# Optimization experiments

Measured on AMD Instinct MI355X. Metric: run time of the kernel, lower is better.

Reference implementation:

```python
import jax, jax.numpy as jnp
import numpy as np

DIM_IN, DIM_OUT, DIM_CTX = 128, 256, 259
B, N, S_CTX = 32, 2048, 1
BN_EPS = 1e-5


def setup_inputs() -> dict:
    key = jax.random.key(0)
    ks = jax.random.split(key, 12)
    s = 0.02
    return {
        "ctx": jax.random.normal(ks[0], (B, S_CTX, DIM_CTX), jnp.float32),
        "x": jax.random.normal(ks[1], (B, N, DIM_IN), jnp.float32),
        "W_layer": jax.random.normal(ks[2], (DIM_OUT, DIM_IN), jnp.float32) * s,
        "b_layer": jax.random.normal(ks[3], (DIM_OUT,), jnp.float32) * s,
        "W_hbias": jax.random.normal(ks[4], (DIM_OUT, DIM_CTX), jnp.float32) * s,
        "W_gate": jax.random.normal(ks[5], (DIM_OUT, DIM_CTX), jnp.float32) * s,
        "b_gate": jax.random.normal(ks[6], (DIM_OUT,), jnp.float32) * s,
        "W_k": jax.random.normal(ks[7], (DIM_OUT, DIM_CTX - 3), jnp.float32) * s,
        "W_v": jax.random.normal(ks[8], (DIM_OUT, DIM_CTX - 3), jnp.float32) * s,
        "W_tc": jax.random.normal(ks[9], (DIM_OUT, DIM_OUT), jnp.float32) * s,
        "b_tc": jax.random.normal(ks[10], (DIM_OUT,), jnp.float32) * s,
        "bn_gamma": jnp.ones((N,), jnp.float32),
        "bn_beta": jnp.zeros((N,), jnp.float32),
    }


def reference(ctx, x, W_layer, b_layer, W_hbias, W_gate, b_gate, W_k, W_v, W_tc, b_tc, bn_gamma, bn_beta):
    # FiLM gate / bias from context: [B, 1, dim_out]
    gate = jax.nn.sigmoid(jnp.einsum('bsc,oc->bso', ctx, W_gate) + b_gate)
    bias = jnp.einsum('bsc,oc->bso', ctx, W_hbias)

    # main linear: [B, N, dim_out]
    x1 = jnp.einsum('bni,oi->bno', x, W_layer) + b_layer

    # channel attention from shape context (drop last 3 ctx dims)
    shape = ctx[:, :, : ctx.shape[2] - 3]                      # [B, S, C-3]
    shape_k = jnp.einsum('bsc,oc->bos', shape, W_k)            # [B, dim_out, S]
    shape_v = jnp.einsum('bsc,oc->bso', shape, W_v)            # [B, S, dim_out]
    energy = jnp.einsum('bos,bse->boe', shape_k, shape_v)      # [B, dim_out, dim_out]
    attention = jax.nn.softmax(energy, axis=-1)
    attention = attention / (1e-9 + attention.sum(axis=1, keepdims=True))

    # channel mixing: [B, N, dim_out]
    x_r = jnp.einsum('bno,boe->bne', x1, attention)

    # trans_conv + BatchNorm1d(N) (train-mode batch stats over dims (0, 2)) + ReLU
    t = jnp.einsum('bno,eo->bne', x1 - x_r, W_tc) + b_tc       # [B, N, dim_out]
    mean = t.mean(axis=(0, 2), keepdims=True)                  # per point-channel
    var = t.var(axis=(0, 2), keepdims=True)                    # biased variance
    t = (t - mean) * jax.lax.rsqrt(var + BN_EPS)
    t = t * bn_gamma[None, :, None] + bn_beta[None, :, None]
    x_r = jax.nn.relu(t)

    xo = x1 + x_r
    return xo * gate + bias
```

## Files before the change

kernel.cpp:

```cpp
#include <hip/hip_runtime.h>
#include <hip/hip_bf16.h>

#define BB   32
#define NN   2048
#define DIN  128
#define DOUT 256
#define DCTX 259

#define OFF_AB   0u
#define OFF_WMB  16777216u
#define OFF_WLB  17301504u
#define OFF_WLTB 17317888u
#define OFF_WTCB 17334272u
#define OFF_G    17367040u
#define OFF_HB   17375232u
#define OFF_TB   17383424u
#define OFF_WKT  17391616u
#define OFF_WVT  17457152u
#define OFF_WGT  17522688u
#define OFF_WHT  17588992u
#define OFF_P1   17655296u
#define OFF_P2   17720832u
#define OFF_SC   17786368u
#define OFF_SH   17788416u

typedef short bf16x8 __attribute__((ext_vector_type(8)));
typedef float f32x4  __attribute__((ext_vector_type(4)));

static __device__ inline unsigned short f2bf(float f) {
    __hip_bfloat16 h = __float2bfloat16(f);
    return *(unsigned short*)&h;
}
static __device__ inline float bf2f(unsigned short u) {
    unsigned v = ((unsigned)u) << 16;
    float f;
    __builtin_memcpy(&f, &v, 4);
    return f;
}

__global__ void kXW(const float* __restrict__ Wl, const float* __restrict__ Wtc,
                    const float* __restrict__ Wk, const float* __restrict__ Wv,
                    const float* __restrict__ Wg, const float* __restrict__ Whb,
                    float* __restrict__ ws) {
    unsigned bb = blockIdx.x, t = threadIdx.x;
    if (bb < 8u) {
        unsigned base = bb * 8192u;
        unsigned short* dst = (unsigned short*)(ws + OFF_WTCB);
#pragma unroll
        for (int j = 0; j < 32; j++) {
            unsigned i = base + (unsigned)j * 256u + t;
            dst[i] = f2bf(Wtc[i]);
        }
    } else if (bb == 8u) {
        unsigned short* dst = (unsigned short*)(ws + OFF_WLTB);
        for (unsigned idx = t; idx < 32768u; idx += 256u) {
            unsigned i = idx >> 8, o = idx & 255u;
            dst[idx] = f2bf(Wl[o * 128u + i]);
        }
    } else if (bb == 9u) {
        unsigned short* dst = (unsigned short*)(ws + OFF_WLB);
        for (unsigned idx = t; idx < 32768u; idx += 256u) dst[idx] = f2bf(Wl[idx]);
    } else {
        unsigned j = bb - 10u;
        const float* src; float* dst; unsigned C, c0;
        if (j < 8u)       { src = Wk;  dst = ws + OFF_WKT; C = 256; c0 = j * 32u; }
        else if (j < 16u) { src = Wv;  dst = ws + OFF_WVT; C = 256; c0 = (j - 8u) * 32u; }
        else if (j < 25u) { src = Wg;  dst = ws + OFF_WGT; C = 259; c0 = (j - 16u) * 32u; }
        else              { src = Whb; dst = ws + OFF_WHT; C = 259; c0 = (j - 25u) * 32u; }
        for (unsigned cc = c0; cc < c0 + 32u && cc < C; cc++)
            dst[cc * 256u + t] = src[t * C + cc];
    }
}

__global__ __launch_bounds__(1024) void kP(const float* __restrict__ ctx,
                                           const float* __restrict__ bg,
                                           float* __restrict__ ws) {
    const int b = blockIdx.x, t = threadIdx.x;
    const int o = t & 255, q = t >> 8;
    __shared__ __align__(16) float cs[260];
    __shared__ __align__(16) float ks[256], vs[256], rms[256], ris[256];
    __shared__ float pm[1024], ps[1024];
    for (int i = t; i < DCTX; i += 1024) cs[i] = ctx[b * DCTX + i];
    __syncthreads();

    {
        const float* WT; int C;
        if (q == 0)      { WT = ws + OFF_WKT; C = 256; }
        else if (q == 1) { WT = ws + OFF_WVT; C = 256; }
        else if (q == 2) { WT = ws + OFF_WGT; C = DCTX; }
        else             { WT = ws + OFF_WHT; C = DCTX; }
        float s = 0.f;
#pragma unroll 8
        for (int c = 0; c < C; c++) s += WT[c * 256 + o] * cs[c];
        if (q == 0)      ks[o] = s;
        else if (q == 1) vs[o] = s;
        else if (q == 2) ws[OFF_G + b * DOUT + o] = 1.f / (1.f + __expf(-(s + bg[o])));
        else             ws[OFF_HB + b * DOUT + o] = s;
    }
    __syncthreads();

    const float ko = ks[o];
    const float4* vs4 = (const float4*)vs;
    float pmax = -1e30f;
#pragma unroll 4
    for (int j = q * 16; j < q * 16 + 16; j++) {
        float4 v = vs4[j];
        pmax = fmaxf(pmax, fmaxf(fmaxf(ko * v.x, ko * v.y), fmaxf(ko * v.z, ko * v.w)));
    }
    pm[q * 256 + o] = pmax;
    __syncthreads();
    float m = fmaxf(fmaxf(pm[o], pm[256 + o]), fmaxf(pm[512 + o], pm[768 + o]));
    float psum = 0.f;
#pragma unroll 4
    for (int j = q * 16; j < q * 16 + 16; j++) {
        float4 v = vs4[j];
        psum += __expf(ko * v.x - m) + __expf(ko * v.y - m)
              + __expf(ko * v.z - m) + __expf(ko * v.w - m);
    }
    ps[q * 256 + o] = psum;
    __syncthreads();
    float ri = 1.f / (ps[o] + ps[256 + o] + ps[512 + o] + ps[768 + o]);
    if (q == 0) { rms[o] = m; ris[o] = ri; }
    __syncthreads();

    const float ve = vs[o];
    float cp = 0.f;
#pragma unroll 4
    for (int o2 = q * 64; o2 < q * 64 + 64; o2++)
        cp += __expf(ks[o2] * ve - rms[o2]) * ris[o2];
    pm[q * 256 + o] = cp;
    __syncthreads();
    float ci = 1.f / (1e-9f + pm[o] + pm[256 + o] + pm[512 + o] + pm[768 + o]);
    unsigned short* Ab = (unsigned short*)(ws + OFF_AB) + (size_t)b * 65536u;
#pragma unroll 4
    for (int o2 = q * 64; o2 < q * 64 + 64; o2++) {
        float a = __expf(ks[o2] * ve - rms[o2]) * ris[o2] * ci;
        Ab[o2 * 256 + o] = f2bf(a);
    }
}

__global__ __launch_bounds__(512) void k45(const float* __restrict__ bl,
                                           const float* __restrict__ btc,
                                           float* __restrict__ ws) {
    const int t = threadIdx.x, wid = t >> 6, l = t & 63;
    const int b = blockIdx.y, et = blockIdx.x;
    const int lrow = l & 15, lk = l >> 4;
    __shared__ unsigned short Mt[128 * 256];
    const unsigned short* Wtcb = (const unsigned short*)(ws + OFF_WTCB);

    {
        const unsigned short* Ab = (const unsigned short*)(ws + OFF_AB) + (size_t)b * 65536u;
        const int sub = wid >> 2, w2 = wid & 3;
        const int rbase = et * 128 + sub * 64 + (w2 & 1) * 32;
        const int colbase = (w2 >> 1) * 128;
        f32x4 acc[2][8];
#pragma unroll
        for (int i = 0; i < 2; i++)
#pragma unroll
            for (int c = 0; c < 8; c++) acc[i][c] = (f32x4){0.f, 0.f, 0.f, 0.f};
        const unsigned short* ar0 = Wtcb + (rbase + lrow) * 256;
#pragma unroll
        for (int kk = 0; kk < 8; kk++) {
            int ko = kk * 32 + lk * 8;
            bf16x8 a0 = *(const bf16x8*)(ar0 + ko);
            bf16x8 a1 = *(const bf16x8*)(ar0 + 16 * 256 + ko);
            bf16x8 bfr[8];
#pragma unroll
            for (int c = 0; c < 8; c++)
                bfr[c] = *(const bf16x8*)(Ab + (colbase + c * 16 + lrow) * 256 + ko);
#pragma unroll
            for (int c = 0; c < 8; c++) {
                acc[0][c] = __builtin_amdgcn_mfma_f32_16x16x32_bf16(a0, bfr[c], acc[0][c], 0, 0, 0);
                acc[1][c] = __builtin_amdgcn_mfma_f32_16x16x32_bf16(a1, bfr[c], acc[1][c], 0, 0, 0);
            }
        }
#pragma unroll
        for (int t2 = 0; t2 < 2; t2++)
#pragma unroll
            for (int c = 0; c < 8; c++)
#pragma unroll
                for (int r = 0; r < 4; r++) {
                    int grow = rbase + t2 * 16 + lk * 4 + r;
                    int col = colbase + c * 16 + lrow;
                    float idv = bf2f(Wtcb[grow * 256 + col]);
                    int rl = grow - et * 128;
                    Mt[rl * 256 + (col ^ ((rl & 7) << 3))] = f2bf(idv - acc[t2][c][r]);
                }
    }
    __syncthreads();
    {
        const unsigned short* Wltb = (const unsigned short*)(ws + OFF_WLTB);
        const int rl0 = wid * 16;
        f32x4 acc[8];
#pragma unroll
        for (int c = 0; c < 8; c++) acc[c] = (f32x4){0.f, 0.f, 0.f, 0.f};
        const int arow = rl0 + lrow;
        const int asw = (arow & 7) << 3;
#pragma unroll
        for (int kk = 0; kk < 8; kk++) {
            int ko = kk * 32 + lk * 8;
            bf16x8 a0 = *(const bf16x8*)(Mt + arow * 256 + (ko ^ asw));
            bf16x8 bfr[8];
#pragma unroll
            for (int c = 0; c < 8; c++)
                bfr[c] = *(const bf16x8*)(Wltb + (c * 16 + lrow) * 256 + ko);
#pragma unroll
            for (int c = 0; c < 8; c++)
                acc[c] = __builtin_amdgcn_mfma_f32_16x16x32_bf16(a0, bfr[c], acc[c], 0, 0, 0);
        }
        unsigned short* WMBp = (unsigned short*)(ws + OFF_WMB) + (size_t)b * 32768u;
#pragma unroll
        for (int c = 0; c < 8; c++)
#pragma unroll
            for (int r = 0; r < 4; r++) {
                int row = et * 128 + rl0 + lk * 4 + r;
                int col = c * 16 + lrow;
                WMBp[row * 128 + col] = f2bf(acc[c][r]);
            }
    }
    if (t < 128) {
        const int rl = t;
        const int sw = (rl & 7) << 3;
        float s = 0.f;
#pragma unroll 4
        for (int j = 0; j < 32; j++) {
            bf16x8 ch = *(const bf16x8*)(Mt + rl * 256 + ((j * 8) ^ sw));
#pragma unroll
            for (int u = 0; u < 8; u++) s += bl[j * 8 + u] * bf2f((unsigned short)ch[u]);
        }
        ws[OFF_TB + b * DOUT + et * 128 + rl] = s + btc[et * 128 + rl];
    }
}

#define LDP 136

__global__ __launch_bounds__(256) void kS(const float* __restrict__ x,
                                          float* __restrict__ ws) {
    const int t = threadIdx.x;
    const int wid = t >> 6, l = t & 63;
    const int b = blockIdx.x, nt = blockIdx.y;
    const int n0 = nt * 64;
    const int lrow = l & 15, lk = l >> 4;
    __shared__ unsigned short xs[64 * LDP];
    __shared__ float sp1[4][64], sp2[4][64];

    const float4* xg = (const float4*)(x + (size_t)(b * NN + n0) * DIN);
#pragma unroll
    for (int it = 0; it < 8; it++) {
        int idx = it * 256 + t;
        int row = idx >> 5, kq = idx & 31;
        float4 v = xg[idx];
        ushort4 u;
        u.x = f2bf(v.x); u.y = f2bf(v.y); u.z = f2bf(v.z); u.w = f2bf(v.w);
        *(ushort4*)(xs + row * LDP + kq * 4) = u;
    }
    __syncthreads();

    const int colbase = wid * 64;
    f32x4 acc[4][4];
#pragma unroll
    for (int rt = 0; rt < 4; rt++)
#pragma unroll
        for (int ct = 0; ct < 4; ct++) acc[rt][ct] = (f32x4){0.f, 0.f, 0.f, 0.f};
    {
        const unsigned short* wb = (const unsigned short*)(ws + OFF_WMB) + (size_t)b * 32768u;
#pragma unroll
        for (int kk = 0; kk < 4; kk++) {
            int ko = kk * 32 + lk * 8;
            bf16x8 a[4];
#pragma unroll
            for (int rt = 0; rt < 4; rt++)
                a[rt] = *(const bf16x8*)(xs + (rt * 16 + lrow) * LDP + ko);
            bf16x8 bf[4];
#pragma unroll
            for (int ct = 0; ct < 4; ct++)
                bf[ct] = *(const bf16x8*)(wb + (size_t)(colbase + ct * 16 + lrow) * DIN + ko);
#pragma unroll
            for (int rt = 0; rt < 4; rt++)
#pragma unroll
                for (int ct = 0; ct < 4; ct++)
                    acc[rt][ct] = __builtin_amdgcn_mfma_f32_16x16x32_bf16(a[rt], bf[ct], acc[rt][ct], 0, 0, 0);
        }
#pragma unroll
        for (int ct = 0; ct < 4; ct++) {
            float bv = ws[OFF_TB + b * DOUT + colbase + ct * 16 + lrow];
#pragma unroll
            for (int rt = 0; rt < 4; rt++)
#pragma unroll
                for (int r = 0; r < 4; r++) acc[rt][ct][r] += bv;
        }
    }

    float s1[4][4], s2[4][4];
#pragma unroll
    for (int rt = 0; rt < 4; rt++)
#pragma unroll
        for (int r = 0; r < 4; r++) { s1[rt][r] = 0.f; s2[rt][r] = 0.f; }
#pragma unroll
    for (int rt = 0; rt < 4; rt++)
#pragma unroll
        for (int ct = 0; ct < 4; ct++)
#pragma unroll
            for (int r = 0; r < 4; r++) {
                float v = acc[rt][ct][r];
                s1[rt][r] += v; s2[rt][r] += v * v;
            }
#pragma unroll
    for (int off = 1; off < 16; off <<= 1) {
#pragma unroll
        for (int rt = 0; rt < 4; rt++)
#pragma unroll
            for (int r = 0; r < 4; r++) {
                s1[rt][r] += __shfl_xor(s1[rt][r], off, 64);
                s2[rt][r] += __shfl_xor(s2[rt][r], off, 64);
            }
    }
    if (lrow == 0) {
#pragma unroll
        for (int rt = 0; rt < 4; rt++)
#pragma unroll
            for (int r = 0; r < 4; r++) {
                int nidx = rt * 16 + lk * 4 + r;
                sp1[wid][nidx] = s1[rt][r];
                sp2[wid][nidx] = s2[rt][r];
            }
    }
    __syncthreads();
    if (t < 64) {
        float S1 = sp1[0][t] + sp1[1][t] + sp1[2][t] + sp1[3][t];
        float S2 = sp2[0][t] + sp2[1][t] + sp2[2][t] + sp2[3][t];
        ws[OFF_P1 + (size_t)b * NN + n0 + t] = S1;
        ws[OFF_P2 + (size_t)b * NN + n0 + t] = S2;
    }
}

__global__ __launch_bounds__(256) void kBN(const float* __restrict__ gamma,
                                           const float* __restrict__ beta,
                                           float* __restrict__ ws) {
    const int n = blockIdx.x * 256 + threadIdx.x;
    float S1 = 0.f, S2 = 0.f;
#pragma unroll 8
    for (int b = 0; b < BB; b++) {
        S1 += ws[OFF_P1 + (size_t)b * NN + n];
        S2 += ws[OFF_P2 + (size_t)b * NN + n];
    }
    float mean = S1 * (1.f / 8192.f);
    float var  = S2 * (1.f / 8192.f) - mean * mean;
    float sc = gamma[n] * rsqrtf(fmaxf(var, 0.f) + 1e-5f);
    ws[OFF_SC + n] = sc;
    ws[OFF_SH + n] = beta[n] - mean * sc;
}

__global__ __launch_bounds__(256, 4) void kF(const float* __restrict__ x,
                                             const float* __restrict__ bl,
                                             float* __restrict__ out,
                                             float* __restrict__ ws) {
    const int t = threadIdx.x;
    const int wid = t >> 6, l = t & 63;
    const int b = blockIdx.x;
    const int nt = blockIdx.y;
    const int n0 = nt * 32;
    const int lrow = l & 15, lk = l >> 4;
    __shared__ unsigned short xs[32 * LDP];
    __shared__ float scs[32], shs[32];

    if (t < 32) {
        scs[t] = ws[OFF_SC + n0 + t];
        shs[t] = ws[OFF_SH + n0 + t];
    }
    const float4* xg = (const float4*)(x + (size_t)(b * NN + n0) * DIN);
#pragma unroll
    for (int it = 0; it < 4; it++) {
        int idx = it * 256 + t;
        int row = idx >> 5, kq = idx & 31;
        float4 v = xg[idx];
        ushort4 u;
        u.x = f2bf(v.x); u.y = f2bf(v.y); u.z = f2bf(v.z); u.w = f2bf(v.w);
        *(ushort4*)(xs + row * LDP + kq * 4) = u;
    }
    __syncthreads();

    const int colbase = wid * 64;

    f32x4 acc[2][4];
#pragma unroll
    for (int rt = 0; rt < 2; rt++)
#pragma unroll
        for (int ct = 0; ct < 4; ct++) acc[rt][ct] = (f32x4){0.f, 0.f, 0.f, 0.f};
    {
        const unsigned short* wb = (const unsigned short*)(ws + OFF_WMB) + (size_t)b * 32768u;
#pragma unroll
        for (int kk = 0; kk < 4; kk++) {
            int ko = kk * 32 + lk * 8;
            bf16x8 a[2];
#pragma unroll
            for (int rt = 0; rt < 2; rt++)
                a[rt] = *(const bf16x8*)(xs + (rt * 16 + lrow) * LDP + ko);
            bf16x8 bf[4];
#pragma unroll
            for (int ct = 0; ct < 4; ct++)
                bf[ct] = *(const bf16x8*)(wb + (size_t)(colbase + ct * 16 + lrow) * DIN + ko);
#pragma unroll
            for (int rt = 0; rt < 2; rt++)
#pragma unroll
                for (int ct = 0; ct < 4; ct++)
                    acc[rt][ct] = __builtin_amdgcn_mfma_f32_16x16x32_bf16(a[rt], bf[ct], acc[rt][ct], 0, 0, 0);
        }
#pragma unroll
        for (int ct = 0; ct < 4; ct++) {
            float bv = ws[OFF_TB + b * DOUT + colbase + ct * 16 + lrow];
#pragma unroll
            for (int rt = 0; rt < 2; rt++)
#pragma unroll
                for (int r = 0; r < 4; r++) acc[rt][ct][r] += bv;
        }
    }

    f32x4 acc0[2][4];
#pragma unroll
    for (int rt = 0; rt < 2; rt++)
#pragma unroll
        for (int ct = 0; ct < 4; ct++) acc0[rt][ct] = (f32x4){0.f, 0.f, 0.f, 0.f};
    {
        const unsigned short* wb = (const unsigned short*)(ws + OFF_WLB);
#pragma unroll
        for (int kk = 0; kk < 4; kk++) {
            int ko = kk * 32 + lk * 8;
            bf16x8 a[2];
#pragma unroll
            for (int rt = 0; rt < 2; rt++)
                a[rt] = *(const bf16x8*)(xs + (rt * 16 + lrow) * LDP + ko);
            bf16x8 bf[4];
#pragma unroll
            for (int ct = 0; ct < 4; ct++)
                bf[ct] = *(const bf16x8*)(wb + (size_t)(colbase + ct * 16 + lrow) * DIN + ko);
#pragma unroll
            for (int rt = 0; rt < 2; rt++)
#pragma unroll
                for (int ct = 0; ct < 4; ct++)
                    acc0[rt][ct] = __builtin_amdgcn_mfma_f32_16x16x32_bf16(a[rt], bf[ct], acc0[rt][ct], 0, 0, 0);
        }
#pragma unroll
        for (int ct = 0; ct < 4; ct++) {
            float bv = bl[colbase + ct * 16 + lrow];
#pragma unroll
            for (int rt = 0; rt < 2; rt++)
#pragma unroll
                for (int r = 0; r < 4; r++) acc0[rt][ct][r] += bv;
        }
    }

    float gv[4], hbv[4];
#pragma unroll
    for (int ct = 0; ct < 4; ct++) {
        int o = colbase + ct * 16 + lrow;
        gv[ct]  = ws[OFF_G  + b * DOUT + o];
        hbv[ct] = ws[OFF_HB + b * DOUT + o];
    }
#pragma unroll
    for (int rt = 0; rt < 2; rt++)
#pragma unroll
        for (int r = 0; r < 4; r++) {
            int nidx = rt * 16 + lk * 4 + r;
            float sc = scs[nidx], sh = shs[nidx];
            int n = n0 + nidx;
#pragma unroll
            for (int ct = 0; ct < 4; ct++) {
                int o = colbase + ct * 16 + lrow;
                float rv = fmaxf(acc[rt][ct][r] * sc + sh, 0.f);
                out[(size_t)((b * NN + n) * DOUT) + o] = (acc0[rt][ct][r] + rv) * gv[ct] + hbv[ct];
            }
        }
}

extern "C" void kernel_launch(void* const* d_in, const int* in_sizes, int n_in,
                              void* d_out, int out_size, void* d_ws, size_t ws_size,
                              hipStream_t stream) {
    const float* ctx   = (const float*)d_in[0];
    const float* x     = (const float*)d_in[1];
    const float* Wl    = (const float*)d_in[2];
    const float* bl    = (const float*)d_in[3];
    const float* Whb   = (const float*)d_in[4];
    const float* Wg    = (const float*)d_in[5];
    const float* bg    = (const float*)d_in[6];
    const float* Wk    = (const float*)d_in[7];
    const float* Wv    = (const float*)d_in[8];
    const float* Wtc   = (const float*)d_in[9];
    const float* btc   = (const float*)d_in[10];
    const float* gamma = (const float*)d_in[11];
    const float* beta  = (const float*)d_in[12];
    float* out = (float*)d_out;
    float* ws  = (float*)d_ws;

    kXW <<<44, 256, 0, stream>>>(Wl, Wtc, Wk, Wv, Wg, Whb, ws);
    kP  <<<BB, 1024, 0, stream>>>(ctx, bg, ws);
    k45 <<<dim3(2, BB), 512, 0, stream>>>(bl, btc, ws);
    kS  <<<dim3(BB, 32), 256, 0, stream>>>(x, ws);
    kBN <<<8, 256, 0, stream>>>(gamma, beta, ws);
    kF  <<<dim3(BB, 64), 256, 0, stream>>>(x, bl, out, ws);
}
```

Baseline: 247.0 us.

## Merge weight-prep into context kernel and fold BN stats into final kernel

Removes the separate weight-transpose kernel by having extra blocks of the context kernel convert Wtc and Wl to bf16. The context projections now read the original row-major weights directly using 16-lane shuffle reductions instead of pre-transposed copies. The BN statistics kernel is removed and its finalize step is recomputed per tile inside the final kernel. The two MFMA loops in the final kernel are interleaved and the x loads are issued earlier. This cuts two launches and their serial dependencies, at the cost of redundant BN reduction work in each of the 32×64 blocks.

After: 271.7 us. 10.0% more time.

```diff
diff --git a/kernel.cpp b/kernel.cpp
--- a/kernel.cpp
+++ b/kernel.cpp
@@ -15,14 +15,8 @@
 #define OFF_G    17367040u
 #define OFF_HB   17375232u
 #define OFF_TB   17383424u
-#define OFF_WKT  17391616u
-#define OFF_WVT  17457152u
-#define OFF_WGT  17522688u
-#define OFF_WHT  17588992u
-#define OFF_P1   17655296u
-#define OFF_P2   17720832u
-#define OFF_SC   17786368u
-#define OFF_SH   17788416u
+#define OFF_P1   17391616u
+#define OFF_P2   17457152u
 
 typedef short bf16x8 __attribute__((ext_vector_type(8)));
 typedef float f32x4  __attribute__((ext_vector_type(4)));
@@ -38,45 +32,36 @@
     return f;
 }
 
-__global__ void kXW(const float* __restrict__ Wl, const float* __restrict__ Wtc,
-                    const float* __restrict__ Wk, const float* __restrict__ Wv,
-                    const float* __restrict__ Wg, const float* __restrict__ Whb,
-                    float* __restrict__ ws) {
-    unsigned bb = blockIdx.x, t = threadIdx.x;
-    if (bb < 8u) {
-        unsigned base = bb * 8192u;
-        unsigned short* dst = (unsigned short*)(ws + OFF_WTCB);
-#pragma unroll
-        for (int j = 0; j < 32; j++) {
-            unsigned i = base + (unsigned)j * 256u + t;
-            dst[i] = f2bf(Wtc[i]);
-        }
-    } else if (bb == 8u) {
-        unsigned short* dst = (unsigned short*)(ws + OFF_WLTB);
-        for (unsigned idx = t; idx < 32768u; idx += 256u) {
-            unsigned i = idx >> 8, o = idx & 255u;
-            dst[idx] = f2bf(Wl[o * 128u + i]);
-        }
-    } else if (bb == 9u) {
-        unsigned short* dst = (unsigned short*)(ws + OFF_WLB);
-        for (unsigned idx = t; idx < 32768u; idx += 256u) dst[idx] = f2bf(Wl[idx]);
-    } else {
-        unsigned j = bb - 10u;
-        const float* src; float* dst; unsigned C, c0;
-        if (j < 8u)       { src = Wk;  dst = ws + OFF_WKT; C = 256; c0 = j * 32u; }
-        else if (j < 16u) { src = Wv;  dst = ws + OFF_WVT; C = 256; c0 = (j - 8u) * 32u; }
-        else if (j < 25u) { src = Wg;  dst = ws + OFF_WGT; C = 259; c0 = (j - 16u) * 32u; }
-        else              { src = Whb; dst = ws + OFF_WHT; C = 259; c0 = (j - 25u) * 32u; }
-        for (unsigned cc = c0; cc < c0 + 32u && cc < C; cc++)
-            dst[cc * 256u + t] = src[t * C + cc];
-    }
-}
-
-__global__ __launch_bounds__(1024) void kP(const float* __restrict__ ctx,
-                                           const float* __restrict__ bg,
-                                           float* __restrict__ ws) {
-    const int b = blockIdx.x, t = threadIdx.x;
+__global__ __launch_bounds__(1024) void kPW(const float* __restrict__ ctx,
+                                            const float* __restrict__ bg,
+                                            const float* __restrict__ Wl,
+                                            const float* __restrict__ Wtc,
+                                            const float* __restrict__ Wk,
+                                            const float* __restrict__ Wv,
+                                            const float* __restrict__ Wg,
+                                            const float* __restrict__ Whb,
+                                            float* __restrict__ ws) {
+    const int bb = blockIdx.x, t = threadIdx.x;
+    if (bb >= BB) {
+        if (bb == BB) {
+            unsigned short* dst = (unsigned short*)(ws + OFF_WTCB);
+            for (int i = t; i < 65536; i += 1024) dst[i] = f2bf(Wtc[i]);
+        } else {
+            unsigned short* d0 = (unsigned short*)(ws + OFF_WLB);
+            unsigned short* d1 = (unsigned short*)(ws + OFF_WLTB);
+            for (int i = t; i < 32768; i += 1024) {
+                float v = Wl[i];
+                d0[i] = f2bf(v);
+                int o = i >> 7, c = i & 127;
+                d1[c * 256 + o] = f2bf(v);
+            }
+        }
+        return;
+    }
+
+    const int b = bb;
     const int o = t & 255, q = t >> 8;
+    const int wid = t >> 6, l = t & 63;
     __shared__ __align__(16) float cs[260];
     __shared__ __align__(16) float ks[256], vs[256], rms[256], ris[256];
     __shared__ float pm[1024], ps[1024];
@@ -84,18 +69,31 @@
     __syncthreads();
 
     {
-        const float* WT; int C;
-        if (q == 0)      { WT = ws + OFF_WKT; C = 256; }
-        else if (q == 1) { WT = ws + OFF_WVT; C = 256; }
-        else if (q == 2) { WT = ws + OFF_WGT; C = DCTX; }
-        else             { WT = ws + OFF_WHT; C = DCTX; }
-        float s = 0.f;
-#pragma unroll 8
-        for (int c = 0; c < C; c++) s += WT[c * 256 + o] * cs[c];
-        if (q == 0)      ks[o] = s;
-        else if (q == 1) vs[o] = s;
-        else if (q == 2) ws[OFF_G + b * DOUT + o] = 1.f / (1.f + __expf(-(s + bg[o])));
-        else             ws[OFF_HB + b * DOUT + o] = s;
+        const int g16 = l >> 4, lane16 = l & 15;
+        const int m = wid >> 2;
+        const float* Wm; int C;
+        if (m == 0)      { Wm = Wk;  C = 256; }
+        else if (m == 1) { Wm = Wv;  C = 256; }
+        else if (m == 2) { Wm = Wg;  C = DCTX; }
+        else             { Wm = Whb; C = DCTX; }
+#pragma unroll 4
+        for (int i = 0; i < 16; i++) {
+            int d = wid * 64 + i * 4 + g16;
+            int oo = d & 255;
+            const float* wr = Wm + (size_t)oo * C;
+            float p = 0.f;
+#pragma unroll
+            for (int j = 0; j < 16; j++) p += wr[lane16 + 16 * j] * cs[lane16 + 16 * j];
+            if (C == DCTX && lane16 < 3) p += wr[256 + lane16] * cs[256 + lane16];
+#pragma unroll
+            for (int off = 1; off < 16; off <<= 1) p += __shfl_xor(p, off, 16);
+            if (lane16 == 0) {
+                if (m == 0)      ks[oo] = p;
+                else if (m == 1) vs[oo] = p;
+                else if (m == 2) ws[OFF_G + b * DOUT + oo] = 1.f / (1.f + __expf(-(p + bg[oo])));
+                else             ws[OFF_HB + b * DOUT + oo] = p;
+            }
+        }
     }
     __syncthreads();
 
@@ -109,18 +107,18 @@
     }
     pm[q * 256 + o] = pmax;
     __syncthreads();
-    float m = fmaxf(fmaxf(pm[o], pm[256 + o]), fmaxf(pm[512 + o], pm[768 + o]));
+    float m2 = fmaxf(fmaxf(pm[o], pm[256 + o]), fmaxf(pm[512 + o], pm[768 + o]));
     float psum = 0.f;
 #pragma unroll 4
     for (int j = q * 16; j < q * 16 + 16; j++) {
         float4 v = vs4[j];
-        psum += __expf(ko * v.x - m) + __expf(ko * v.y - m)
-              + __expf(ko * v.z - m) + __expf(ko * v.w - m);
+        psum += __expf(ko * v.x - m2) + __expf(ko * v.y - m2)
+              + __expf(ko * v.z - m2) + __expf(ko * v.w - m2);
     }
     ps[q * 256 + o] = psum;
     __syncthreads();
     float ri = 1.f / (ps[o] + ps[256 + o] + ps[512 + o] + ps[768 + o]);
-    if (q == 0) { rms[o] = m; ris[o] = ri; }
+    if (q == 0) { rms[o] = m2; ris[o] = ri; }
     __syncthreads();
 
     const float ve = vs[o];
@@ -334,25 +332,10 @@
     }
 }
 
-__global__ __launch_bounds__(256) void kBN(const float* __restrict__ gamma,
-                                           const float* __restrict__ beta,
-                                           float* __restrict__ ws) {
-    const int n = blockIdx.x * 256 + threadIdx.x;
-    float S1 = 0.f, S2 = 0.f;
-#pragma unroll 8
-    for (int b = 0; b < BB; b++) {
-        S1 += ws[OFF_P1 + (size_t)b * NN + n];
-        S2 += ws[OFF_P2 + (size_t)b * NN + n];
-    }
-    float mean = S1 * (1.f / 8192.f);
-    float var  = S2 * (1.f / 8192.f) - mean * mean;
-    float sc = gamma[n] * rsqrtf(fmaxf(var, 0.f) + 1e-5f);
-    ws[OFF_SC + n] = sc;
-    ws[OFF_SH + n] = beta[n] - mean * sc;
-}
-
 __global__ __launch_bounds__(256, 4) void kF(const float* __restrict__ x,
                                              const float* __restrict__ bl,
+                                             const float* __restrict__ gamma,
+                                             const float* __restrict__ beta,
                                              float* __restrict__ out,
                                              float* __restrict__ ws) {
     const int t = threadIdx.x;
@@ -364,89 +347,81 @@
     __shared__ unsigned short xs[32 * LDP];
     __shared__ float scs[32], shs[32];
 
+    const float4* xg = (const float4*)(x + (size_t)(b * NN + n0) * DIN);
+    float4 xv[4];
+#pragma unroll
+    for (int it = 0; it < 4; it++) xv[it] = xg[it * 256 + t];
+
     if (t < 32) {
-        scs[t] = ws[OFF_SC + n0 + t];
-        shs[t] = ws[OFF_SH + n0 + t];
-    }
-    const float4* xg = (const float4*)(x + (size_t)(b * NN + n0) * DIN);
+        float S1 = 0.f, S2 = 0.f;
+#pragma unroll 8
+        for (int b2 = 0; b2 < BB; b2++) {
+            S1 += ws[OFF_P1 + (size_t)b2 * NN + n0 + t];
+            S2 += ws[OFF_P2 + (size_t)b2 * NN + n0 + t];
+        }
+        float mean = S1 * (1.f / 8192.f);
+        float var  = S2 * (1.f / 8192.f) - mean * mean;
+        float sc = gamma[n0 + t] * rsqrtf(fmaxf(var, 0.f) + 1e-5f);
+        scs[t] = sc;
+        shs[t] = beta[n0 + t] - mean * sc;
+    }
 #pragma unroll
     for (int it = 0; it < 4; it++) {
         int idx = it * 256 + t;
         int row = idx >> 5, kq = idx & 31;
-        float4 v = xg[idx];
         ushort4 u;
-        u.x = f2bf(v.x); u.y = f2bf(v.y); u.z = f2bf(v.z); u.w = f2bf(v.w);
+        u.x = f2bf(xv[it].x); u.y = f2bf(xv[it].y); u.z = f2bf(xv[it].z); u.w = f2bf(xv[it].w);
         *(ushort4*)(xs + row * LDP + kq * 4) = u;
     }
     __syncthreads();
 
     const int colbase = wid * 64;
 
-    f32x4 acc[2][4];
+    f32x4 acc[2][4], acc0[2][4];
 #pragma unroll
     for (int rt = 0; rt < 2; rt++)
 #pragma unroll
-        for (int ct = 0; ct < 4; ct++) acc[rt][ct] = (f32x4){0.f, 0.f, 0.f, 0.f};
+        for (int ct = 0; ct < 4; ct++) {
+            acc[rt][ct]  = (f32x4){0.f, 0.f, 0.f, 0.f};
+            acc0[rt][ct] = (f32x4){0.f, 0.f, 0.f, 0.f};
+        }
     {
-        const unsigned short* wb = (const unsigned short*)(ws + OFF_WMB) + (size_t)b * 32768u;
+        const unsigned short* wbM = (const unsigned short*)(ws + OFF_WMB) + (size_t)b * 32768u;
+        const unsigned short* wbL = (const unsigned short*)(ws + OFF_WLB);
 #pragma unroll
         for (int kk = 0; kk < 4; kk++) {
             int ko = kk * 32 + lk * 8;
-            bf16x8 a[2];
+            bf16x8 a0 = *(const bf16x8*)(xs + lrow * LDP + ko);
+            bf16x8 a1 = *(const bf16x8*)(xs + (16 + lrow) * LDP + ko);
+            bf16x8 bf[4];
+#pragma unroll
+            for (int ct = 0; ct < 4; ct++)
+                bf[ct] = *(const bf16x8*)(wbM + (size_t)(colbase + ct * 16 + lrow) * DIN + ko);
+#pragma unroll
+            for (int ct = 0; ct < 4; ct++) {
+                acc[0][ct] = __builtin_amdgcn_mfma_f32_16x16x32_bf16(a0, bf[ct], acc[0][ct], 0, 0, 0);
+                acc[1][ct] = __builtin_amdgcn_mfma_f32_16x16x32_bf16(a1, bf[ct], acc[1][ct], 0, 0, 0);
+            }
+#pragma unroll
+            for (int ct = 0; ct < 4; ct++)
+                bf[ct] = *(const bf16x8*)(wbL + (size_t)(colbase + ct * 16 + lrow) * DIN + ko);
+#pragma unroll
+            for (int ct = 0; ct < 4; ct++) {
+                acc0[0][ct] = __builtin_amdgcn_mfma_f32_16x16x32_bf16(a0, bf[ct], acc0[0][ct], 0, 0, 0);
+                acc0[1][ct] = __builtin_amdgcn_mfma_f32_16x16x32_bf16(a1, bf[ct], acc0[1][ct], 0, 0, 0);
+            }
+        }
+#pragma unroll
+        for (int ct = 0; ct < 4; ct++) {
+            float bvM = ws[OFF_TB + b * DOUT + colbase + ct * 16 + lrow];
+            float bvL = bl[colbase + ct * 16 + lrow];
 #pragma unroll
             for (int rt = 0; rt < 2; rt++)
-                a[rt] = *(const bf16x8*)(xs + (rt * 16 + lrow) * LDP + ko);
-            bf16x8 bf[4];
-#pragma unroll
-            for (int ct = 0; ct < 4; ct++)
-                bf[ct] = *(const bf16x8*)(wb + (size_t)(colbase + ct * 16 + lrow) * DIN + ko);
-#pragma unroll
-            for (int rt = 0; rt < 2; rt++)
-#pragma unroll
-                for (int ct = 0; ct < 4; ct++)
-                    acc[rt][ct] = __builtin_amdgcn_mfma_f32_16x16x32_bf16(a[rt], bf[ct], acc[rt][ct], 0, 0, 0);
-        }
-#pragma unroll
-        for (int ct = 0; ct < 4; ct++) {
-            float bv = ws[OFF_TB + b * DOUT + colbase + ct * 16 + lrow];
-#pragma unroll
-            for (int rt = 0; rt < 2; rt++)
-#pragma unroll
-                for (int r = 0; r < 4; r++) acc[rt][ct][r] += bv;
-        }
-    }
-
-    f32x4 acc0[2][4];
-#pragma unroll
-    for (int rt = 0; rt < 2; rt++)
-#pragma unroll
-        for (int ct = 0; ct < 4; ct++) acc0[rt][ct] = (f32x4){0.f, 0.f, 0.f, 0.f};
-    {
-        const unsigned short* wb = (const unsigned short*)(ws + OFF_WLB);
-#pragma unroll
-        for (int kk = 0; kk < 4; kk++) {
-            int ko = kk * 32 + lk * 8;
-            bf16x8 a[2];
-#pragma unroll
-            for (int rt = 0; rt < 2; rt++)
-                a[rt] = *(const bf16x8*)(xs + (rt * 16 + lrow) * LDP + ko);
-            bf16x8 bf[4];
-#pragma unroll
-            for (int ct = 0; ct < 4; ct++)
-                bf[ct] = *(const bf16x8*)(wb + (size_t)(colbase + ct * 16 + lrow) * DIN + ko);
-#pragma unroll
-            for (int rt = 0; rt < 2; rt++)
-#pragma unroll
-                for (int ct = 0; ct < 4; ct++)
-                    acc0[rt][ct] = __builtin_amdgcn_mfma_f32_16x16x32_bf16(a[rt], bf[ct], acc0[rt][ct], 0, 0, 0);
-        }
-#pragma unroll
-        for (int ct = 0; ct < 4; ct++) {
-            float bv = bl[colbase + ct * 16 + lrow];
-#pragma unroll
-            for (int rt = 0; rt < 2; rt++)
-#pragma unroll
-                for (int r = 0; r < 4; r++) acc0[rt][ct][r] += bv;
+#pragma unroll
+                for (int r = 0; r < 4; r++) {
+                    acc[rt][ct][r]  += bvM;
+                    acc0[rt][ct][r] += bvL;
+                }
         }
     }
 
@@ -492,10 +467,8 @@
     float* out = (float*)d_out;
     float* ws  = (float*)d_ws;
 
-    kXW <<<44, 256, 0, stream>>>(Wl, Wtc, Wk, Wv, Wg, Whb, ws);
-    kP  <<<BB, 1024, 0, stream>>>(ctx, bg, ws);
+    kPW <<<34, 1024, 0, stream>>>(ctx, bg, Wl, Wtc, Wk, Wv, Wg, Whb, ws);
     k45 <<<dim3(2, BB), 512, 0, stream>>>(bl, btc, ws);
     kS  <<<dim3(BB, 32), 256, 0, stream>>>(x, ws);
-    kBN <<<8, 256, 0, stream>>>(gamma, beta, ws);
-    kF  <<<dim3(BB, 64), 256, 0, stream>>>(x, bl, out, ws);
-}
+    kF  <<<dim3(BB, 64), 256, 0, stream>>>(x, bl, gamma, beta, out, ws);
+}
```

## Fuse BatchNorm stat finalize into final kernel and double its row tile

Applied to the files above, without the earlier changes.

Removes the separate kBN launch. Each final-kernel block now reduces the per-batch partial sums for its own 64 points and computes scale and shift itself. The block tile grows from 32 to 64 rows, which halves the grid and halves reloads of the per-batch weights. The two GEMMs are merged into one k-loop, and the x loads are issued before the BN reduction so their latency overlaps. The cost is more registers per thread (launch bounds drop to 2 blocks per SM) and the BN reduction being repeated across the 32 batch blocks.

Measured after the change: 239.7 us. 1.03x faster.

```diff
diff --git a/kernel.cpp b/kernel.cpp
--- a/kernel.cpp
+++ b/kernel.cpp
@@ -21,8 +21,6 @@
 #define OFF_WHT  17588992u
 #define OFF_P1   17655296u
 #define OFF_P2   17720832u
-#define OFF_SC   17786368u
-#define OFF_SH   17788416u
 
 typedef short bf16x8 __attribute__((ext_vector_type(8)));
 typedef float f32x4  __attribute__((ext_vector_type(4)));
@@ -334,119 +332,98 @@
     }
 }
 
-__global__ __launch_bounds__(256) void kBN(const float* __restrict__ gamma,
-                                           const float* __restrict__ beta,
-                                           float* __restrict__ ws) {
-    const int n = blockIdx.x * 256 + threadIdx.x;
-    float S1 = 0.f, S2 = 0.f;
-#pragma unroll 8
-    for (int b = 0; b < BB; b++) {
-        S1 += ws[OFF_P1 + (size_t)b * NN + n];
-        S2 += ws[OFF_P2 + (size_t)b * NN + n];
-    }
-    float mean = S1 * (1.f / 8192.f);
-    float var  = S2 * (1.f / 8192.f) - mean * mean;
-    float sc = gamma[n] * rsqrtf(fmaxf(var, 0.f) + 1e-5f);
-    ws[OFF_SC + n] = sc;
-    ws[OFF_SH + n] = beta[n] - mean * sc;
-}
-
-__global__ __launch_bounds__(256, 4) void kF(const float* __restrict__ x,
+__global__ __launch_bounds__(256, 2) void kF(const float* __restrict__ x,
                                              const float* __restrict__ bl,
+                                             const float* __restrict__ gamma,
+                                             const float* __restrict__ beta,
                                              float* __restrict__ out,
                                              float* __restrict__ ws) {
     const int t = threadIdx.x;
     const int wid = t >> 6, l = t & 63;
     const int b = blockIdx.x;
     const int nt = blockIdx.y;
-    const int n0 = nt * 32;
+    const int n0 = nt * 64;
     const int lrow = l & 15, lk = l >> 4;
-    __shared__ unsigned short xs[32 * LDP];
-    __shared__ float scs[32], shs[32];
-
-    if (t < 32) {
-        scs[t] = ws[OFF_SC + n0 + t];
-        shs[t] = ws[OFF_SH + n0 + t];
-    }
+    __shared__ unsigned short xs[64 * LDP];
+    __shared__ float scs[64], shs[64];
+
     const float4* xg = (const float4*)(x + (size_t)(b * NN + n0) * DIN);
-#pragma unroll
-    for (int it = 0; it < 4; it++) {
+    float4 xv[8];
+#pragma unroll
+    for (int it = 0; it < 8; it++) xv[it] = xg[it * 256 + t];
+
+    if (t < 64) {
+        float S1 = 0.f, S2 = 0.f;
+#pragma unroll 8
+        for (int b2 = 0; b2 < BB; b2++) {
+            S1 += ws[OFF_P1 + (size_t)b2 * NN + n0 + t];
+            S2 += ws[OFF_P2 + (size_t)b2 * NN + n0 + t];
+        }
+        float mean = S1 * (1.f / 8192.f);
+        float var  = S2 * (1.f / 8192.f) - mean * mean;
+        float sc = gamma[n0 + t] * rsqrtf(fmaxf(var, 0.f) + 1e-5f);
+        scs[t] = sc;
+        shs[t] = beta[n0 + t] - mean * sc;
+    }
+#pragma unroll
+    for (int it = 0; it < 8; it++) {
         int idx = it * 256 + t;
         int row = idx >> 5, kq = idx & 31;
-        float4 v = xg[idx];
         ushort4 u;
-        u.x = f2bf(v.x); u.y = f2bf(v.y); u.z = f2bf(v.z); u.w = f2bf(v.w);
+        u.x = f2bf(xv[it].x); u.y = f2bf(xv[it].y); u.z = f2bf(xv[it].z); u.w = f2bf(xv[it].w);
         *(ushort4*)(xs + row * LDP + kq * 4) = u;
     }
     __syncthreads();
 
     const int colbase = wid * 64;
 
-    f32x4 acc[2][4];
-#pragma unroll
-    for (int rt = 0; rt < 2; rt++)
-#pragma unroll
-        for (int ct = 0; ct < 4; ct++) acc[rt][ct] = (f32x4){0.f, 0.f, 0.f, 0.f};
+    f32x4 acc[4][4], acc0[4][4];
+#pragma unroll
+    for (int rt = 0; rt < 4; rt++)
+#pragma unroll
+        for (int ct = 0; ct < 4; ct++) {
+            acc[rt][ct]  = (f32x4){0.f, 0.f, 0.f, 0.f};
+            acc0[rt][ct] = (f32x4){0.f, 0.f, 0.f, 0.f};
+        }
     {
-        const unsigned short* wb = (const unsigned short*)(ws + OFF_WMB) + (size_t)b * 32768u;
+        const unsigned short* wbM = (const unsigned short*)(ws + OFF_WMB) + (size_t)b * 32768u;
+        const unsigned short* wbL = (const unsigned short*)(ws + OFF_WLB);
 #pragma unroll
         for (int kk = 0; kk < 4; kk++) {
             int ko = kk * 32 + lk * 8;
-            bf16x8 a[2];
-#pragma unroll
-            for (int rt = 0; rt < 2; rt++)
+            bf16x8 a[4];
+#pragma unroll
+            for (int rt = 0; rt < 4; rt++)
                 a[rt] = *(const bf16x8*)(xs + (rt * 16 + lrow) * LDP + ko);
             bf16x8 bf[4];
 #pragma unroll
             for (int ct = 0; ct < 4; ct++)
-                bf[ct] = *(const bf16x8*)(wb + (size_t)(colbase + ct * 16 + lrow) * DIN + ko);
-#pragma unroll
-            for (int rt = 0; rt < 2; rt++)
+                bf[ct] = *(const bf16x8*)(wbM + (size_t)(colbase + ct * 16 + lrow) * DIN + ko);
+#pragma unroll
+            for (int rt = 0; rt < 4; rt++)
 #pragma unroll
                 for (int ct = 0; ct < 4; ct++)
                     acc[rt][ct] = __builtin_amdgcn_mfma_f32_16x16x32_bf16(a[rt], bf[ct], acc[rt][ct], 0, 0, 0);
-        }
-#pragma unroll
-        for (int ct = 0; ct < 4; ct++) {
-            float bv = ws[OFF_TB + b * DOUT + colbase + ct * 16 + lrow];
-#pragma unroll
-            for (int rt = 0; rt < 2; rt++)
-#pragma unroll
-                for (int r = 0; r < 4; r++) acc[rt][ct][r] += bv;
-        }
-    }
-
-    f32x4 acc0[2][4];
-#pragma unroll
-    for (int rt = 0; rt < 2; rt++)
-#pragma unroll
-        for (int ct = 0; ct < 4; ct++) acc0[rt][ct] = (f32x4){0.f, 0.f, 0.f, 0.f};
-    {
-        const unsigned short* wb = (const unsigned short*)(ws + OFF_WLB);
-#pragma unroll
-        for (int kk = 0; kk < 4; kk++) {
-            int ko = kk * 32 + lk * 8;
-            bf16x8 a[2];
-#pragma unroll
-            for (int rt = 0; rt < 2; rt++)
-                a[rt] = *(const bf16x8*)(xs + (rt * 16 + lrow) * LDP + ko);
-            bf16x8 bf[4];
 #pragma unroll
             for (int ct = 0; ct < 4; ct++)
-                bf[ct] = *(const bf16x8*)(wb + (size_t)(colbase + ct * 16 + lrow) * DIN + ko);
-#pragma unroll
-            for (int rt = 0; rt < 2; rt++)
+                bf[ct] = *(const bf16x8*)(wbL + (size_t)(colbase + ct * 16 + lrow) * DIN + ko);
+#pragma unroll
+            for (int rt = 0; rt < 4; rt++)
 #pragma unroll
                 for (int ct = 0; ct < 4; ct++)
                     acc0[rt][ct] = __builtin_amdgcn_mfma_f32_16x16x32_bf16(a[rt], bf[ct], acc0[rt][ct], 0, 0, 0);
         }
 #pragma unroll
         for (int ct = 0; ct < 4; ct++) {
-            float bv = bl[colbase + ct * 16 + lrow];
-#pragma unroll
-            for (int rt = 0; rt < 2; rt++)
-#pragma unroll
-                for (int r = 0; r < 4; r++) acc0[rt][ct][r] += bv;
+            float bvM = ws[OFF_TB + b * DOUT + colbase + ct * 16 + lrow];
+            float bvL = bl[colbase + ct * 16 + lrow];
+#pragma unroll
+            for (int rt = 0; rt < 4; rt++)
+#pragma unroll
+                for (int r = 0; r < 4; r++) {
+                    acc[rt][ct][r]  += bvM;
+                    acc0[rt][ct][r] += bvL;
+                }
         }
     }
 
@@ -458,7 +435,7 @@
         hbv[ct] = ws[OFF_HB + b * DOUT + o];
     }
 #pragma unroll
-    for (int rt = 0; rt < 2; rt++)
+    for (int rt = 0; rt < 4; rt++)
 #pragma unroll
         for (int r = 0; r < 4; r++) {
             int nidx = rt * 16 + lk * 4 + r;
@@ -496,6 +473,5 @@
     kP  <<<BB, 1024, 0, stream>>>(ctx, bg, ws);
     k45 <<<dim3(2, BB), 512, 0, stream>>>(bl, btc, ws);
     kS  <<<dim3(BB, 32), 256, 0, stream>>>(x, ws);
-    kBN <<<8, 256, 0, stream>>>(gamma, beta, ws);
-    kF  <<<dim3(BB, 64), 256, 0, stream>>>(x, bl, out, ws);
-}
+    kF  <<<dim3(BB, 32), 256, 0, stream>>>(x, bl, gamma, beta, out, ws);
+}
```
